# Performance work log

Hardware: AMD Instinct MI355X
Metric: run time of the kernel (lower is better)

## Reference

```python
import jax, jax.numpy as jnp
import numpy as np

B, SQ, SK, D = 8, 512, 512, 32


def _spd_cov(key, b, s, d):
    # random SPD covariance: A A^T + I
    a = 0.1 * jax.random.normal(key, (b, s, d, d), dtype=jnp.float32)
    return jnp.einsum('bsde,bsfe->bsdf', a, a) + jnp.eye(d, dtype=jnp.float32)


def setup_inputs() -> dict:
    key = jax.random.key(0)
    ks = jax.random.split(key, 6)
    return {
        'q_mean': jax.random.normal(ks[0], (B, SQ, D), dtype=jnp.float32),
        'q_cov': _spd_cov(ks[1], B, SQ, D),
        'k_mean': jax.random.normal(ks[2], (B, SK, D), dtype=jnp.float32),
        'k_cov': _spd_cov(ks[3], B, SK, D),
        'v_mean': jax.random.normal(ks[4], (B, SK, D), dtype=jnp.float32),
        'v_cov': _spd_cov(ks[5], B, SK, D),
    }


def reference(q_mean, q_cov, k_mean, k_cov, v_mean, v_cov):
    # Pairwise symmetric Gaussian JSD attention.
    # JSD = 0.5*(KL(p_q||p_k)+KL(p_k||p_q)); the log-det terms cancel:
    # JSD = 0.25*( tr(Sk^-1 Sq) + tr(Sq^-1 Sk) - 2D
    #              + dm^T (Sk^-1 + Sq^-1) dm ),  dm = mu_q - mu_k
    d = q_mean.shape[-1]
    q_inv = jnp.linalg.inv(q_cov)            # [B,Sq,D,D]
    k_inv = jnp.linalg.inv(k_cov)            # [B,Sk,D,D]
    tr_kq = jnp.einsum('bkde,bqed->bqk', k_inv, q_cov)
    tr_qk = jnp.einsum('bqde,bked->bqk', q_inv, k_cov)
    dm = q_mean[:, :, None, :] - k_mean[:, None, :, :]   # [B,Sq,Sk,D]
    quad = (jnp.einsum('bqkd,bkde,bqke->bqk', dm, k_inv, dm)
            + jnp.einsum('bqkd,bqde,bqke->bqk', dm, q_inv, dm))
    js = 0.25 * (tr_kq + tr_qk - 2.0 * d + quad)         # [B,Sq,Sk]
    score = jax.nn.softmax(js, axis=-1)
    out_mean = jnp.einsum('bqk,bkd->bqd', score, v_mean)
    out_cov = jnp.einsum('bqk,bkde->bqde', score, v_cov)
    return out_mean, out_cov
```

## Files before the change

### kernel.cpp

```cpp
#include <hip/hip_runtime.h>
#include <hip/hip_bf16.h>

#define NBATCH 8
#define SQL 512
#define SKL 512
#define DD 32
#define KF 1152
#define UT 528
#define NOUT 1056
#define NVT 1088
#define NSITE (NBATCH * SQL)
#define FEAT_BLOCKS (2 * NSITE / 4)
#define VS_BLOCKS (34 * 16 * NBATCH)

typedef short short8 __attribute__((ext_vector_type(8)));
typedef float f32x4 __attribute__((ext_vector_type(4)));
typedef unsigned short ushort_t;

__device__ __forceinline__ ushort_t f2bf(float f) {
    unsigned int u = __float_as_uint(f);
    return (ushort_t)((u + 0x7fffu + ((u >> 16) & 1u)) >> 16);
}
__device__ __forceinline__ float bf2f(ushort_t h) {
    return __uint_as_float(((unsigned int)h) << 16);
}
__device__ __forceinline__ float rdlane(float x, int l) {
    return __int_as_float(__builtin_amdgcn_readlane(__float_as_int(x), l));
}
__device__ __forceinline__ void gl_lds16(const ushort_t* g, ushort_t* l) {
    __builtin_amdgcn_global_load_lds(
        (const __attribute__((address_space(1))) void*)g,
        (__attribute__((address_space(3))) void*)l, 16, 0, 0);
}
__device__ __forceinline__ void pk_split(float v0, float v1, ushort_t& h0, ushort_t& h1,
                                         ushort_t& l0, ushort_t& l1) {
    __hip_bfloat162 H = __float22bfloat162_rn(make_float2(v0, v1));
    ushort2 hu = *(ushort2*)&H;
    h0 = hu.x; h1 = hu.y;
    __hip_bfloat162 L = __float22bfloat162_rn(make_float2(v0 - bf2f(hu.x), v1 - bf2f(hu.y)));
    ushort2 lu = *(ushort2*)&L;
    l0 = lu.x; l1 = lu.y;
}

__global__ __launch_bounds__(256, 8) void feat_kernel(
    const float* __restrict__ qm, const float* __restrict__ qc,
    const float* __restrict__ km, const float* __restrict__ kc,
    ushort_t* __restrict__ fqh, ushort_t* __restrict__ fql,
    ushort_t* __restrict__ fkh, ushort_t* __restrict__ fkl)
{
    __shared__ float smem[4 * 624];
    const int wid = threadIdx.x >> 6;
    const int lane = threadIdx.x & 63;
    const int gsite = blockIdx.x * 4 + wid;
    const int qside = gsite < NSITE;
    const int site = qside ? gsite : gsite - NSITE;

    const float* mean = qside ? qm : km;
    const float* cov  = qside ? qc : kc;
    ushort_t* fh = qside ? fqh : fkh;
    ushort_t* fl = qside ? fql : fkl;

    const float* covp = cov + (size_t)site * (DD * DD);
    const float* mup  = mean + (size_t)site * DD;
    const size_t fo = (size_t)site * KF;

    float* inv_p = smem + wid * 624;
    float* mu_s  = inv_p + 560;
    float* iv_s  = mu_s + 32;

    if (lane < DD) mu_s[lane] = mup[lane];

    float a[DD];
    if (lane < DD) {
        #pragma unroll
        for (int r = 0; r < DD; ++r) a[r] = covp[r * DD + lane];
    } else {
        const int c = lane - DD;
        #pragma unroll
        for (int r = 0; r < DD; ++r) a[r] = (r == c) ? 1.0f : 0.0f;
    }

    #pragma unroll
    for (int p = 0; p < DD; ++p) {
        float piv = rdlane(a[p], p);
        float rinv = 1.0f / piv;
        float t = a[p] * rinv;
        #pragma unroll
        for (int r = 0; r < DD; ++r) {
            if (r != p) {
                float fr = rdlane(a[r], p);
                a[r] = fmaf(-fr, t, a[r]);
            }
        }
        a[p] = t;
    }

    if (lane >= DD) {
        const int c = lane - DD;
        #pragma unroll
        for (int r = 0; r < DD; ++r)
            if (r <= c) inv_p[((r * (65 - r)) >> 1) + (c - r)] = a[r];
    }
    __syncthreads();

    {
        const int j = lane & 31;
        const int basej = (j * (65 - j)) >> 1;
        float s = 0.f;
        #pragma unroll
        for (int e = 0; e < DD; ++e) {
            const int be = (e * (65 - e)) >> 1;
            const int addr = (e < j) ? (be + (j - e)) : (basej + (e - j));
            s += inv_p[addr] * mu_s[e];
        }
        if (lane < DD) iv_s[lane] = s;
    }
    __syncthreads();

    float bias = 0.f;
    #pragma unroll
    for (int d2 = 0; d2 < DD; ++d2) bias += mu_s[d2] * iv_s[d2];

    for (int idx = lane; idx < UT; idx += 64) {
        int d = (int)((65.0f - sqrtf(4225.0f - 8.0f * (float)idx)) * 0.5f);
        if (d > 0 && (d * (65 - d)) / 2 > idx) --d;
        if (((d + 1) * (64 - d)) / 2 <= idx) ++d;
        int off = (d * (65 - d)) / 2;
        int e = d + (idx - off);
        float Mv = covp[d * DD + e] + mu_s[d] * mu_s[e];
        float Iv = inv_p[idx];
        float w = (d == e) ? 0.25f : 0.5f;
        float v0, v1;
        if (qside) { v0 = w * Mv; v1 = w * Iv; }
        else       { v0 = Iv;     v1 = Mv; }
        ushort_t h0, h1, l0, l1;
        pk_split(v0, v1, h0, h1, l0, l1);
        fh[fo + idx] = h0; fh[fo + UT + idx] = h1;
        fl[fo + idx] = l0; fl[fo + UT + idx] = l1;
    }
    if (lane < DD) {
        float ivv = iv_s[lane], muv = mu_s[lane];
        float v0, v1;
        if (qside) { v0 = -0.5f * ivv; v1 = 0.25f * muv; }
        else       { v0 = muv;         v1 = -2.f * ivv; }
        ushort_t h0, h1, l0, l1;
        pk_split(v0, v1, h0, h1, l0, l1);
        fh[fo + 2*UT + lane] = h0; fh[fo + 2*UT + DD + lane] = h1;
        fl[fo + 2*UT + lane] = l0; fl[fo + 2*UT + DD + lane] = l1;
    }
    if (lane == 32) {
        float v = qside ? 0.25f : bias;
        ushort_t hb = f2bf(v);
        fh[fo + 2*UT + 2*DD] = hb;
        fl[fo + 2*UT + 2*DD] = f2bf(v - bf2f(hb));
    }
    for (int i = 2*UT + 2*DD + 1 + lane; i < KF; i += 64) { fh[fo + i] = 0; fl[fo + i] = 0; }
}

template<int MODE>
__global__ __launch_bounds__(256) void gemm_split(
    const ushort_t* __restrict__ Ah_g, const ushort_t* __restrict__ Al_g,
    const ushort_t* __restrict__ Bh_g, const ushort_t* __restrict__ Bl_g,
    float* __restrict__ C0, float* __restrict__ C1)
{
    constexpr bool SPLIT = (MODE == 0);
    constexpr int KSTRIDE = SPLIT ? KF : SKL;
    constexpr int KITERS = SPLIT ? (KF / 2 / 32) : (SKL / 32);
    const int b = blockIdx.z, nt = blockIdx.x;
    const int mt = SPLIT ? (blockIdx.y & 3) : blockIdx.y;
    const int kbase = SPLIT ? ((blockIdx.y >> 2) * (KF / 2)) : 0;
    const int tid = threadIdx.x, lane = tid & 63, wid = tid >> 6;
    const int wm = wid & 1, wn = wid >> 1;
    const int BROWS = MODE ? NVT : SKL;

    const ushort_t* Ah = Ah_g + ((size_t)b * SQL + mt * 128) * KSTRIDE;
    const ushort_t* Al = Al_g + ((size_t)b * SQL + mt * 128) * KSTRIDE;
    const ushort_t* Bh = Bh_g + ((size_t)b * BROWS + nt * 64) * KSTRIDE;
    const ushort_t* Bl = Bl_g + ((size_t)b * BROWS + nt * 64) * KSTRIDE;

    __shared__ __align__(16) ushort_t AsH[128 * 32];
    __shared__ __align__(16) ushort_t AsL[SPLIT ? 128 * 32 : 8];
    __shared__ __align__(16) ushort_t BsH[64 * 32];
    __shared__ __align__(16) ushort_t BsL[SPLIT ? 64 * 32 : 8];

    const int r4 = lane >> 2, kp = (lane & 3) * 8;
    const int arow0 = wid * 16 + r4,        aoff0 = wid * 512 + lane * 8;
    const int arow1 = (wid + 4) * 16 + r4,  aoff1 = (wid + 4) * 512 + lane * 8;

    const int fm = lane & 15;
    const int q8 = (lane >> 4) * 8;

    f32x4 acc[4][2];
    #pragma unroll
    for (int i = 0; i < 4; ++i)
        #pragma unroll
        for (int j = 0; j < 2; ++j)
            acc[i][j] = (f32x4){0.f, 0.f, 0.f, 0.f};

    for (int it = 0; it < KITERS; ++it) {
        const int k0 = kbase + it * 32;
        __syncthreads();
        gl_lds16(Ah + (size_t)arow0 * KSTRIDE + k0 + kp, &AsH[aoff0]);
        gl_lds16(Ah + (size_t)arow1 * KSTRIDE + k0 + kp, &AsH[aoff1]);
        gl_lds16(Bh + (size_t)arow0 * KSTRIDE + k0 + kp, &BsH[aoff0]);
        if (SPLIT) {
            gl_lds16(Al + (size_t)arow0 * KSTRIDE + k0 + kp, &AsL[aoff0]);
            gl_lds16(Al + (size_t)arow1 * KSTRIDE + k0 + kp, &AsL[aoff1]);
            gl_lds16(Bl + (size_t)arow0 * KSTRIDE + k0 + kp, &BsL[aoff0]);
        }
        __syncthreads();

        short8 ah[4], al[4], bh[2], bl[2];
        #pragma unroll
        for (int i = 0; i < 4; ++i) {
            const int r = wm * 64 + i * 16 + fm;
            ah[i] = *(const short8*)&AsH[r * 32 + q8];
            if (SPLIT) al[i] = *(const short8*)&AsL[r * 32 + q8];
        }
        #pragma unroll
        for (int j = 0; j < 2; ++j) {
            const int r = wn * 32 + j * 16 + fm;
            bh[j] = *(const short8*)&BsH[r * 32 + q8];
            if (SPLIT) bl[j] = *(const short8*)&BsL[r * 32 + q8];
        }
        #pragma unroll
        for (int i = 0; i < 4; ++i)
            #pragma unroll
            for (int j = 0; j < 2; ++j) {
                acc[i][j] = __builtin_amdgcn_mfma_f32_16x16x32_bf16(ah[i], bh[j], acc[i][j], 0, 0, 0);
                if (SPLIT) {
                    acc[i][j] = __builtin_amdgcn_mfma_f32_16x16x32_bf16(ah[i], bl[j], acc[i][j], 0, 0, 0);
                    acc[i][j] = __builtin_amdgcn_mfma_f32_16x16x32_bf16(al[i], bh[j], acc[i][j], 0, 0, 0);
                }
            }
    }

    const int crow0 = (lane >> 4) * 4;
    const int ccol = lane & 15;
    #pragma unroll
    for (int i = 0; i < 4; ++i) {
        const int m = mt * 128 + wm * 64 + i * 16 + crow0;
        #pragma unroll
        for (int j = 0; j < 2; ++j) {
            const int n = nt * 64 + wn * 32 + j * 16 + ccol;
            #pragma unroll
            for (int r = 0; r < 4; ++r) {
                const float v = acc[i][j][r];
                const size_t rowb = (size_t)b * SQL + (m + r);
                if (MODE == 0) {
                    atomicAdd(&C0[rowb * SKL + n], v);
                } else {
                    if (n < DD)        C0[rowb * DD + n] = v;
                    else if (n < NOUT) C1[rowb * (DD * DD) + (n - DD)] = v;
                }
            }
        }
    }
}

__global__ __launch_bounds__(256) void phase2_kernel(
    const float* __restrict__ js, ushort_t* __restrict__ ph,
    const float* __restrict__ vmean, const float* __restrict__ vcov,
    ushort_t* __restrict__ vth)
{
    __shared__ float sm[32 * 33];
    const int tid = threadIdx.x;
    if (blockIdx.x < (unsigned)(NBATCH * SQL)) {
        const float* p = js + (size_t)blockIdx.x * SKL;
        float2 v = *(const float2*)(p + 2 * tid);
        float m = fmaxf(v.x, v.y);
        #pragma unroll
        for (int o = 32; o > 0; o >>= 1) m = fmaxf(m, __shfl_xor(m, o));
        const int wid = tid >> 6, ln = tid & 63;
        if (ln == 0) sm[wid] = m;
        __syncthreads();
        m = fmaxf(fmaxf(sm[0], sm[1]), fmaxf(sm[2], sm[3]));
        float e0 = __expf(v.x - m), e1 = __expf(v.y - m);
        float s = e0 + e1;
        #pragma unroll
        for (int o = 32; o > 0; o >>= 1) s += __shfl_xor(s, o);
        if (ln == 0) sm[4 + wid] = s;
        __syncthreads();
        s = sm[4] + sm[5] + sm[6] + sm[7];
        float rs = 1.0f / s;
        size_t o = (size_t)blockIdx.x * SKL + 2 * tid;
        ph[o]     = f2bf(e0 * rs);
        ph[o + 1] = f2bf(e1 * rs);
    } else {
        const int vb = blockIdx.x - NBATCH * SQL;
        const int b = vb / (34 * 16), rem = vb % (34 * 16);
        const int kt = rem / 34, nt = rem % 34;
        const int n0 = nt * 32, k0 = kt * 32;
        const int tx = tid & 31, ty = tid >> 5;
        for (int r = ty; r < 32; r += 8) {
            const int k = k0 + r, n = n0 + tx;
            float v;
            if (n0 == 0)          v = vmean[((size_t)b * SKL + k) * DD + n];
            else if (n0 >= NOUT)  v = 0.f;
            else                  v = vcov[((size_t)b * SKL + k) * (DD * DD) + (n - DD)];
            sm[tx * 33 + r] = v;
        }
        __syncthreads();
        for (int r = ty; r < 32; r += 8) {
            const int n = n0 + r, k = k0 + tx;
            vth[((size_t)b * NVT + n) * SKL + k] = f2bf(sm[r * 33 + tx]);
        }
    }
}

extern "C" void kernel_launch(void* const* d_in, const int* in_sizes, int n_in,
                              void* d_out, int out_size, void* d_ws, size_t ws_size,
                              hipStream_t stream)
{
    const float* q_mean = (const float*)d_in[0];
    const float* q_cov  = (const float*)d_in[1];
    const float* k_mean = (const float*)d_in[2];
    const float* k_cov  = (const float*)d_in[3];
    const float* v_mean = (const float*)d_in[4];
    const float* v_cov  = (const float*)d_in[5];

    float* out_mean = (float*)d_out;
    float* out_cov  = out_mean + (size_t)NBATCH * SQL * DD;

    char* w = (char*)d_ws;
    const size_t FQN = (size_t)NBATCH * SQL * KF;
    ushort_t* fq_h = (ushort_t*)w;
    ushort_t* fq_l = fq_h + FQN;
    ushort_t* fk_h = fq_l + FQN;
    ushort_t* fk_l = fk_h + FQN;
    float*    js   = (float*)(fk_l + FQN);
    ushort_t* vt_h = fq_h;
    ushort_t* p_h  = fk_h;

    feat_kernel<<<FEAT_BLOCKS, 256, 0, stream>>>(
        q_mean, q_cov, k_mean, k_cov, fq_h, fq_l, fk_h, fk_l);
    hipMemsetAsync(js, 0, (size_t)NBATCH * SQL * SKL * sizeof(float), stream);
    gemm_split<0><<<dim3(SKL / 64, 8, NBATCH), 256, 0, stream>>>(
        fq_h, fq_l, fk_h, fk_l, js, nullptr);
    phase2_kernel<<<NBATCH * SQL + VS_BLOCKS, 256, 0, stream>>>(
        js, p_h, v_mean, v_cov, vt_h);
    gemm_split<1><<<dim3(NVT / 64, SQL / 128, NBATCH), 256, 0, stream>>>(
        p_h, nullptr, vt_h, nullptr, out_mean, out_cov);
}
```

Baseline: 218.0 us.

## Invert two covariances per wavefront with in-place Gauss-Jordan via ds_swizzle

The feature kernel now processes two sites per wavefront, one per 32-lane half, instead of one site per wavefront with an augmented identity in the upper lanes. Each half runs an in-place Gauss-Jordan inversion that broadcasts pivot values with ds_swizzle instead of readlane, and uses the hardware reciprocal. The inverse is stored as a padded full matrix, and the inverse-times-mean and bias are computed from registers with a swizzle reduction, which drops two block barriers. The goal is to halve the inversion work per site and cut launch and synchronisation overhead, at the cost of more shared memory per block, a lower occupancy hint, a less precise reciprocal and no pivoting.

After: 190.3 us. 1.15x faster.

```diff
diff --git a/kernel.cpp b/kernel.cpp
--- a/kernel.cpp
+++ b/kernel.cpp
@@ -10,7 +10,6 @@
 #define NOUT 1056
 #define NVT 1088
 #define NSITE (NBATCH * SQL)
-#define FEAT_BLOCKS (2 * NSITE / 4)
 #define VS_BLOCKS (34 * 16 * NBATCH)
 
 typedef short short8 __attribute__((ext_vector_type(8)));
@@ -23,9 +22,6 @@
 }
 __device__ __forceinline__ float bf2f(ushort_t h) {
     return __uint_as_float(((unsigned int)h) << 16);
-}
-__device__ __forceinline__ float rdlane(float x, int l) {
-    return __int_as_float(__builtin_amdgcn_readlane(__float_as_int(x), l));
 }
 __device__ __forceinline__ void gl_lds16(const ushort_t* g, ushort_t* l) {
     __builtin_amdgcn_global_load_lds(
@@ -42,93 +38,91 @@
     l0 = lu.x; l1 = lu.y;
 }
 
-__global__ __launch_bounds__(256, 8) void feat_kernel(
+template<int P>
+__device__ __forceinline__ float swzb(float x) {
+    return __int_as_float(__builtin_amdgcn_ds_swizzle(__float_as_int(x), (P << 5)));
+}
+template<int M>
+__device__ __forceinline__ float swzx(float x) {
+    return __int_as_float(__builtin_amdgcn_ds_swizzle(__float_as_int(x), (M << 10) | 0x1F));
+}
+
+template<int P>
+__device__ __forceinline__ void gj_step(float (&a)[DD], int hl) {
+    float piv = swzb<P>(a[P]);
+    float rinv = __builtin_amdgcn_rcpf(piv);
+    float t = a[P] * rinv;
+    bool isp = (hl == P);
+    float u = isp ? rinv : t;
+    float g = isp ? 0.0f : 1.0f;
+    #pragma unroll
+    for (int i = 0; i < DD; ++i) {
+        if (i == P) continue;
+        float ci = swzb<P>(a[i]);
+        a[i] = fmaf(a[i], g, -(ci * u));
+    }
+    a[P] = u;
+}
+template<int P>
+__device__ __forceinline__ void gj_run(float (&a)[DD], int hl) {
+    gj_step<P>(a, hl);
+    if constexpr (P + 1 < DD) gj_run<P + 1>(a, hl);
+}
+
+__global__ __launch_bounds__(256, 4) void feat_kernel(
     const float* __restrict__ qm, const float* __restrict__ qc,
     const float* __restrict__ km, const float* __restrict__ kc,
     ushort_t* __restrict__ fqh, ushort_t* __restrict__ fql,
     ushort_t* __restrict__ fkh, ushort_t* __restrict__ fkl)
 {
-    __shared__ float smem[4 * 624];
-    const int wid = threadIdx.x >> 6;
-    const int lane = threadIdx.x & 63;
-    const int gsite = blockIdx.x * 4 + wid;
-    const int qside = gsite < NSITE;
-    const int site = qside ? gsite : gsite - NSITE;
-
-    const float* mean = qside ? qm : km;
-    const float* cov  = qside ? qc : kc;
+    __shared__ float inv2[8 * 1064];
+    __shared__ float mu2[8 * 32];
+
+    const int tid = threadIdx.x;
+    const int wid = tid >> 6, lane = tid & 63;
+    const int half = lane >> 5, hl = lane & 31;
+    const int site_g = (blockIdx.x * 4 + wid) * 2 + half;
+    const int qside = site_g < NSITE;
+    const int site = qside ? site_g : site_g - NSITE;
+
+    const float* covp = (qside ? qc : kc) + (size_t)site * (DD * DD);
+    const float* mup  = (qside ? qm : km) + (size_t)site * DD;
     ushort_t* fh = qside ? fqh : fkh;
     ushort_t* fl = qside ? fql : fkl;
-
-    const float* covp = cov + (size_t)site * (DD * DD);
-    const float* mup  = mean + (size_t)site * DD;
     const size_t fo = (size_t)site * KF;
 
-    float* inv_p = smem + wid * 624;
-    float* mu_s  = inv_p + 560;
-    float* iv_s  = mu_s + 32;
-
-    if (lane < DD) mu_s[lane] = mup[lane];
+    float* inv_s = inv2 + (wid * 2 + half) * 1064;
+    float* mu_s  = mu2 + (wid * 2 + half) * 32;
+
+    const float mu_lane = mup[hl];
+    mu_s[hl] = mu_lane;
 
     float a[DD];
-    if (lane < DD) {
-        #pragma unroll
-        for (int r = 0; r < DD; ++r) a[r] = covp[r * DD + lane];
-    } else {
-        const int c = lane - DD;
-        #pragma unroll
-        for (int r = 0; r < DD; ++r) a[r] = (r == c) ? 1.0f : 0.0f;
-    }
-
-    #pragma unroll
-    for (int p = 0; p < DD; ++p) {
-        float piv = rdlane(a[p], p);
-        float rinv = 1.0f / piv;
-        float t = a[p] * rinv;
-        #pragma unroll
-        for (int r = 0; r < DD; ++r) {
-            if (r != p) {
-                float fr = rdlane(a[r], p);
-                a[r] = fmaf(-fr, t, a[r]);
-            }
-        }
-        a[p] = t;
-    }
-
-    if (lane >= DD) {
-        const int c = lane - DD;
-        #pragma unroll
-        for (int r = 0; r < DD; ++r)
-            if (r <= c) inv_p[((r * (65 - r)) >> 1) + (c - r)] = a[r];
-    }
-    __syncthreads();
-
-    {
-        const int j = lane & 31;
-        const int basej = (j * (65 - j)) >> 1;
-        float s = 0.f;
-        #pragma unroll
-        for (int e = 0; e < DD; ++e) {
-            const int be = (e * (65 - e)) >> 1;
-            const int addr = (e < j) ? (be + (j - e)) : (basej + (e - j));
-            s += inv_p[addr] * mu_s[e];
-        }
-        if (lane < DD) iv_s[lane] = s;
-    }
-    __syncthreads();
-
-    float bias = 0.f;
-    #pragma unroll
-    for (int d2 = 0; d2 < DD; ++d2) bias += mu_s[d2] * iv_s[d2];
-
-    for (int idx = lane; idx < UT; idx += 64) {
+    #pragma unroll
+    for (int r = 0; r < DD; ++r) a[r] = covp[r * DD + hl];
+
+    gj_run<0>(a, hl);
+
+    #pragma unroll
+    for (int r = 0; r < DD; ++r) inv_s[r * 33 + hl] = a[r];
+
+    float ivr = 0.f;
+    #pragma unroll
+    for (int e = 0; e < DD; ++e) ivr = fmaf(a[e], mu_s[e], ivr);
+
+    float pb = mu_lane * ivr;
+    pb += swzx<1>(pb); pb += swzx<2>(pb); pb += swzx<4>(pb);
+    pb += swzx<8>(pb); pb += swzx<16>(pb);
+    const float bias = pb;
+
+    for (int idx = hl; idx < UT; idx += 32) {
         int d = (int)((65.0f - sqrtf(4225.0f - 8.0f * (float)idx)) * 0.5f);
         if (d > 0 && (d * (65 - d)) / 2 > idx) --d;
         if (((d + 1) * (64 - d)) / 2 <= idx) ++d;
         int off = (d * (65 - d)) / 2;
         int e = d + (idx - off);
         float Mv = covp[d * DD + e] + mu_s[d] * mu_s[e];
-        float Iv = inv_p[idx];
+        float Iv = inv_s[d * 33 + e];
         float w = (d == e) ? 0.25f : 0.5f;
         float v0, v1;
         if (qside) { v0 = w * Mv; v1 = w * Iv; }
@@ -138,23 +132,22 @@
         fh[fo + idx] = h0; fh[fo + UT + idx] = h1;
         fl[fo + idx] = l0; fl[fo + UT + idx] = l1;
     }
-    if (lane < DD) {
-        float ivv = iv_s[lane], muv = mu_s[lane];
+    {
         float v0, v1;
-        if (qside) { v0 = -0.5f * ivv; v1 = 0.25f * muv; }
-        else       { v0 = muv;         v1 = -2.f * ivv; }
+        if (qside) { v0 = -0.5f * ivr; v1 = 0.25f * mu_lane; }
+        else       { v0 = mu_lane;     v1 = -2.f * ivr; }
         ushort_t h0, h1, l0, l1;
         pk_split(v0, v1, h0, h1, l0, l1);
-        fh[fo + 2*UT + lane] = h0; fh[fo + 2*UT + DD + lane] = h1;
-        fl[fo + 2*UT + lane] = l0; fl[fo + 2*UT + DD + lane] = l1;
-    }
-    if (lane == 32) {
+        fh[fo + 2*UT + hl] = h0; fh[fo + 2*UT + DD + hl] = h1;
+        fl[fo + 2*UT + hl] = l0; fl[fo + 2*UT + DD + hl] = l1;
+    }
+    if (hl == 0) {
         float v = qside ? 0.25f : bias;
         ushort_t hb = f2bf(v);
         fh[fo + 2*UT + 2*DD] = hb;
         fl[fo + 2*UT + 2*DD] = f2bf(v - bf2f(hb));
     }
-    for (int i = 2*UT + 2*DD + 1 + lane; i < KF; i += 64) { fh[fo + i] = 0; fl[fo + i] = 0; }
+    for (int i = 2*UT + 2*DD + 1 + hl; i < KF; i += 32) { fh[fo + i] = 0; fl[fo + i] = 0; }
 }
 
 template<int MODE>
@@ -332,7 +325,7 @@
     ushort_t* vt_h = fq_h;
     ushort_t* p_h  = fk_h;
 
-    feat_kernel<<<FEAT_BLOCKS, 256, 0, stream>>>(
+    feat_kernel<<<2 * NSITE / 8, 256, 0, stream>>>(
         q_mean, q_cov, k_mean, k_cov, fq_h, fq_l, fk_h, fk_l);
     hipMemsetAsync(js, 0, (size_t)NBATCH * SQL * SKL * sizeof(float), stream);
     gemm_split<0><<<dim3(SKL / 64, 8, NBATCH), 256, 0, stream>>>(
```
